# Optimization experiments

Hardware: AMD Instinct MI355X
Metric: run time of the kernel (lower is better)

The kernel has to match this reference:

```python
import jax, jax.numpy as jnp
import numpy as np

B, N, D, E, FF_MULT = 2, 1024, 1024, 8, 4
H = D * FF_MULT


def setup_inputs() -> dict:
    key = jax.random.key(0)
    k = jax.random.split(key, 6)
    tokens = jax.random.normal(k[0], (B, N, D), dtype=jnp.float32)
    # uniform(0,1): strictly positive -> every expert processes every token
    dispatch_weights = jax.random.uniform(k[1], (B, N, E), dtype=jnp.float32)
    combine_weights = jax.random.uniform(k[2], (B, N, E), dtype=jnp.float32)
    # per-expert SwiGLU params, stacked on leading expert axis.
    # stored pre-transposed: y = x @ W  (torch Linear weight is [out,in])
    xavier_dh = np.sqrt(2.0 / (D + H))
    Wg = jax.random.normal(k[3], (E, D, H), dtype=jnp.float32) * xavier_dh
    Wv = jax.random.normal(k[4], (E, D, H), dtype=jnp.float32) * xavier_dh
    Wo = jax.random.normal(k[5], (E, H, D), dtype=jnp.float32) * (0.02 * xavier_dh)
    scale = jnp.full((E,), 1.0 / E, dtype=jnp.float32)  # output_scale init 1/E
    return {"tokens": tokens, "dispatch_weights": dispatch_weights,
            "combine_weights": combine_weights, "Wg": Wg, "Wv": Wv,
            "Wo": Wo, "scale": scale}


def reference(tokens, dispatch_weights, combine_weights, Wg, Wv, Wo, scale):
    b, n, d = tokens.shape
    x = tokens.reshape(b * n, d)                      # (T, D)
    disp = dispatch_weights.reshape(b * n, E)         # (T, E)
    comb = combine_weights.reshape(b * n, E)          # (T, E)
    # SwiGLU FFN for all experts at once (dense grouped GEMM)
    gate = jax.nn.gelu(jnp.einsum('td,edh->teh', x, Wg), approximate=False)
    value = jnp.einsum('td,edh->teh', x, Wv)
    expert_out = jnp.einsum('teh,ehd->ted', gate * value, Wo)  # (T, E, D)
    expert_out = expert_out * scale[None, :, None]
    # combine: weight by combine_weights where dispatched (dispatch > 0)
    w = jnp.where(disp > 0, comb, 0.0)                # (T, E)
    output = jnp.einsum('ted,te->td', expert_out, w)
    return output.reshape(b, n, d)
```

## Files before the change

### kernel.cpp

```cpp
#include <hip/hip_runtime.h>
#include <math.h>

#define T_TOK 2048
#define DDIM 1024
#define HDIM 4096
#define NEXP 8
#define NPRIME 8192
#define KTOT (NEXP * HDIM)
#define NSPLIT 8

typedef unsigned short u16;
typedef __attribute__((ext_vector_type(4))) float f32x4;
typedef __attribute__((ext_vector_type(8))) __bf16 bf16x8;
typedef __attribute__((ext_vector_type(8))) unsigned short u16x8;
typedef __attribute__((ext_vector_type(4))) unsigned short u16x4;

__device__ __forceinline__ u16 f2bf(float f) {
  unsigned int u = __builtin_bit_cast(unsigned int, f);
  u += 0x7fffu + ((u >> 16) & 1u);
  return (u16)(u >> 16);
}

__device__ __forceinline__ void stage16(const u16* g, u16* l) {
  __builtin_amdgcn_global_load_lds((__attribute__((address_space(1))) void*)g,
                                   (__attribute__((address_space(3))) void*)l,
                                   16, 0, 0);
}

__global__ void cvt_x_kernel(const float* __restrict__ x, u16* __restrict__ xb) {
  int i = (blockIdx.x * 256 + threadIdx.x) * 8;
  float4 a = *(const float4*)(x + i);
  float4 b = *(const float4*)(x + i + 4);
  u16x8 o;
  o[0] = f2bf(a.x); o[1] = f2bf(a.y); o[2] = f2bf(a.z); o[3] = f2bf(a.w);
  o[4] = f2bf(b.x); o[5] = f2bf(b.y); o[6] = f2bf(b.z); o[7] = f2bf(b.w);
  *(u16x8*)(xb + i) = o;
}

__global__ void transpose_all_kernel(const float* __restrict__ Wg,
                                     const float* __restrict__ Wv,
                                     const float* __restrict__ Wo,
                                     u16* __restrict__ wgvT, u16* __restrict__ woT2) {
  __shared__ float lds[64][65];
  const int bid = blockIdx.x;
  const int e = bid / 3072;
  const int r = bid % 3072;
  const int which = r >> 10;
  const int tt = r & 1023;
  const float* src; int R, C;
  if (which == 2) { src = Wo + (size_t)e * HDIM * DDIM; R = HDIM; C = DDIM; }
  else            { src = (which ? Wv : Wg) + (size_t)e * DDIM * HDIM; R = DDIM; C = HDIM; }
  const int nrt = R >> 6;
  const int r0 = (tt % nrt) << 6, c0 = (tt / nrt) << 6;
  const int tid = threadIdx.x;
#pragma unroll
  for (int i = 0; i < 4; ++i) {
    int f4 = tid + 256 * i;
    int row = f4 >> 4, c4 = (f4 & 15) << 2;
    float4 v = *(const float4*)(src + (size_t)(r0 + row) * C + c0 + c4);
    lds[row][c4] = v.x; lds[row][c4 + 1] = v.y; lds[row][c4 + 2] = v.z; lds[row][c4 + 3] = v.w;
  }
  __syncthreads();
#pragma unroll
  for (int i = 0; i < 4; ++i) {
    int f4 = tid + 256 * i;
    int cc = f4 >> 4, r4 = (f4 & 15) << 2;
    u16x4 o;
    o[0] = f2bf(lds[r4][cc]);     o[1] = f2bf(lds[r4 + 1][cc]);
    o[2] = f2bf(lds[r4 + 2][cc]); o[3] = f2bf(lds[r4 + 3][cc]);
    u16* dst;
    if (which == 2) {
      dst = woT2 + (size_t)(c0 + cc) * KTOT + e * HDIM + r0 + r4;
    } else {
      int h = c0 + cc;
      int rowp = ((h >> 4) << 5) + which * 16 + (h & 15);
      dst = wgvT + (size_t)e * NPRIME * DDIM + (size_t)rowp * DDIM + r0 + r4;
    }
    *(u16x4*)dst = o;
  }
}


template<int KS>
__device__ __forceinline__ void stageA_half(const u16* Ab, int Am0, int tk,
                                            u16* slot, int tid, int h) {
#pragma unroll
  for (int i = 0; i < 2; ++i) {
    int ca = tid + i * 512;
    int rowi = ca >> 3, sl = ca & 7;
    int row = (rowi & 63) + h * 64 + (rowi >> 6) * 128;
    const u16* g = Ab + (size_t)(Am0 + row) * KS + tk + ((sl ^ (row & 7)) << 3);
    stage16(g, slot + ((row << 3) + sl) * 8);
  }
}
template<int KS>
__device__ __forceinline__ void stageB_full(const u16* Bb, int Bn0, int tk,
                                            u16* slot, int tid) {
#pragma unroll
  for (int i = 0; i < 4; ++i) {
    int cb = tid + i * 512;
    int row = cb >> 3, sl = cb & 7;
    const u16* g = Bb + (size_t)(Bn0 + row) * KS + tk + ((sl ^ (row & 7)) << 3);
    stage16(g, slot + 16384 + cb * 8);
  }
}

__device__ __forceinline__ bf16x8 ldsA(const u16* slot, int row, int j, int lkq) {
  int sl = ((j << 2) | lkq) ^ (row & 7);
  return *(const bf16x8*)(slot + row * 64 + sl * 8);
}
__device__ __forceinline__ bf16x8 ldsB(const u16* slot, int row, int j, int lkq) {
  int sl = ((j << 2) | lkq) ^ (row & 7);
  return *(const bf16x8*)(slot + 16384 + row * 64 + sl * 8);
}

template<int KS>
__device__ __forceinline__ void gemm_loop(const u16* Ab, const u16* Bb,
                                          int Am0, int Bn0, int kbase, int NT,
                                          u16* lds, int tid, f32x4 (&acc)[8][4]) {
  const int lane = tid & 63;
  const int wave = tid >> 6;
  const int wm = wave >> 2;
  const int wn = wave & 3;
  const int l15 = lane & 15;
  const int lkq = lane >> 4;

  u16* slot0 = lds;
  u16* slot1 = lds + 32768;

  stageA_half<KS>(Ab, Am0, kbase, slot0, tid, 0);
  stageA_half<KS>(Ab, Am0, kbase, slot0, tid, 1);
  stageB_full<KS>(Bb, Bn0, kbase, slot0, tid);
  stageA_half<KS>(Ab, Am0, kbase + 64, slot1, tid, 0);
  asm volatile("s_waitcnt vmcnt(2)" ::: "memory");
  asm volatile("s_barrier" ::: "memory");

#pragma unroll 1
  for (int t = 0; t < NT; ++t) {
    u16* s  = lds + (t & 1) * 32768;
    u16* s2 = lds + ((t & 1) ^ 1) * 32768;
    bf16x8 af[4], bfr[2][4];

    if (t + 1 < NT) {
      stageA_half<KS>(Ab, Am0, kbase + (t + 1) * 64, s2, tid, 1);
      stageB_full<KS>(Bb, Bn0, kbase + (t + 1) * 64, s2, tid);
    }
#pragma unroll
    for (int mf = 0; mf < 4; ++mf) af[mf] = ldsA(s, wm * 128 + mf * 16 + l15, 0, lkq);
#pragma unroll
    for (int nf = 0; nf < 4; ++nf) bfr[0][nf] = ldsB(s, wn * 64 + nf * 16 + l15, 0, lkq);
    __builtin_amdgcn_s_setprio(1);
#pragma unroll
    for (int mf = 0; mf < 4; ++mf)
#pragma unroll
      for (int nf = 0; nf < 4; ++nf)
        acc[mf][nf] = __builtin_amdgcn_mfma_f32_16x16x32_bf16(af[mf], bfr[0][nf], acc[mf][nf], 0, 0, 0);
    __builtin_amdgcn_s_setprio(0);
    asm volatile("s_barrier" ::: "memory");

#pragma unroll
    for (int mf = 0; mf < 4; ++mf) af[mf] = ldsA(s, wm * 128 + 64 + mf * 16 + l15, 0, lkq);
    __builtin_amdgcn_s_setprio(1);
#pragma unroll
    for (int mf = 0; mf < 4; ++mf)
#pragma unroll
      for (int nf = 0; nf < 4; ++nf)
        acc[4 + mf][nf] = __builtin_amdgcn_mfma_f32_16x16x32_bf16(af[mf], bfr[0][nf], acc[4 + mf][nf], 0, 0, 0);
    __builtin_amdgcn_s_setprio(0);
    asm volatile("s_barrier" ::: "memory");

#pragma unroll
    for (int mf = 0; mf < 4; ++mf) af[mf] = ldsA(s, wm * 128 + mf * 16 + l15, 1, lkq);
#pragma unroll
    for (int nf = 0; nf < 4; ++nf) bfr[1][nf] = ldsB(s, wn * 64 + nf * 16 + l15, 1, lkq);
    __builtin_amdgcn_s_setprio(1);
#pragma unroll
    for (int mf = 0; mf < 4; ++mf)
#pragma unroll
      for (int nf = 0; nf < 4; ++nf)
        acc[mf][nf] = __builtin_amdgcn_mfma_f32_16x16x32_bf16(af[mf], bfr[1][nf], acc[mf][nf], 0, 0, 0);
    __builtin_amdgcn_s_setprio(0);
    asm volatile("s_barrier" ::: "memory");

    if (t + 2 < NT) stageA_half<KS>(Ab, Am0, kbase + (t + 2) * 64, s, tid, 0);
#pragma unroll
    for (int mf = 0; mf < 4; ++mf) af[mf] = ldsA(s, wm * 128 + 64 + mf * 16 + l15, 1, lkq);
    __builtin_amdgcn_s_setprio(1);
#pragma unroll
    for (int mf = 0; mf < 4; ++mf)
#pragma unroll
      for (int nf = 0; nf < 4; ++nf)
        acc[4 + mf][nf] = __builtin_amdgcn_mfma_f32_16x16x32_bf16(af[mf], bfr[1][nf], acc[4 + mf][nf], 0, 0, 0);
    __builtin_amdgcn_s_setprio(0);
    if (t + 2 < NT)       { asm volatile("s_waitcnt vmcnt(2)" ::: "memory"); }
    else if (t + 2 == NT) { asm volatile("s_waitcnt vmcnt(0)" ::: "memory"); }
    asm volatile("s_barrier" ::: "memory");
  }
}

__global__ void __launch_bounds__(512, 2)
gemm_gv_kernel(const u16* __restrict__ xb, const u16* __restrict__ wgvT,
               const float* __restrict__ disp, const float* __restrict__ comb,
               const float* __restrict__ scale, u16* __restrict__ h) {
  __shared__ u16 lds[65536];

  const int bid = blockIdx.x;
  const int wg = (bid & 7) * 256 + (bid >> 3);
  const int e  = wg >> 8;
  const int rr = wg & 255;
  const int nt = rr >> 3;
  const int mt = rr & 7;

  const int tid = threadIdx.x;
  const int lane = tid & 63;
  const int wave = tid >> 6;
  const int wm = wave >> 2, wn = wave & 3;
  const int l15 = lane & 15, lkq = lane >> 4;

  const u16* Bb = wgvT + (size_t)e * NPRIME * DDIM;
  const int Am0 = mt * 256;
  const int Bn0 = nt * 256;

  f32x4 acc[8][4] = {};
  gemm_loop<DDIM>(xb, Bb, Am0, Bn0, 0, DDIM / 64, lds, tid, acc);

  const float s_e = scale[e];
  const int hbase = nt * 128 + wn * 32;
#pragma unroll
  for (int a = 0; a < 8; ++a) {
#pragma unroll
    for (int r = 0; r < 4; ++r) {
      const int t = Am0 + wm * 128 + a * 16 + lkq * 4 + r;
      const float dv = disp[t * NEXP + e];
      const float cv = comb[t * NEXP + e];
      const float s = (dv > 0.0f) ? cv * s_e : 0.0f;
#pragma unroll
      for (int jj = 0; jj < 2; ++jj) {
        const float g = acc[a][2 * jj][r];
        const float v = acc[a][2 * jj + 1][r];
        const float ge = 0.5f * g * (1.0f + erff(g * 0.70710678f));
        h[(size_t)t * KTOT + e * HDIM + hbase + jj * 16 + l15] = f2bf(ge * v * s);
      }
    }
  }
}

__global__ void __launch_bounds__(512, 2)
gemm_out_kernel(const u16* __restrict__ hb, const u16* __restrict__ woT2,
                float* __restrict__ P) {
  __shared__ u16 lds[65536];

  const int bid = blockIdx.x;
  const int wg = (bid & 7) * 32 + (bid >> 3);
  const int kz = wg >> 5;
  const int rr = wg & 31;
  const int nt = rr >> 3;
  const int mt = rr & 7;

  const int tid = threadIdx.x;
  const int lane = tid & 63;
  const int wave = tid >> 6;
  const int wm = wave >> 2, wn = wave & 3;
  const int l15 = lane & 15, lkq = lane >> 4;

  const int Am0 = mt * 256;
  const int Bn0 = nt * 256;
  const int kbase = kz * (KTOT / NSPLIT);

  f32x4 acc[8][4] = {};
  gemm_loop<KTOT>(hb, woT2, Am0, Bn0, kbase, (KTOT / NSPLIT) / 64, lds, tid, acc);

  float* Pp = P + (size_t)kz * (T_TOK * DDIM);
#pragma unroll
  for (int a = 0; a < 8; ++a) {
#pragma unroll
    for (int r = 0; r < 4; ++r) {
      const int t = Am0 + wm * 128 + a * 16 + lkq * 4 + r;
#pragma unroll
      for (int nf = 0; nf < 4; ++nf)
        Pp[(size_t)t * DDIM + Bn0 + wn * 64 + nf * 16 + l15] = acc[a][nf][r];
    }
  }
}

__global__ void reduce_out_kernel(const float* __restrict__ P, float* __restrict__ out) {
  int i = blockIdx.x * 256 + threadIdx.x;
  float4 a = ((const float4*)P)[i];
#pragma unroll
  for (int s = 1; s < NSPLIT; ++s) {
    float4 b = ((const float4*)P)[i + s * (T_TOK * DDIM / 4)];
    a.x += b.x; a.y += b.y; a.z += b.z; a.w += b.w;
  }
  ((float4*)out)[i] = a;
}

extern "C" void kernel_launch(void* const* d_in, const int* in_sizes, int n_in,
                              void* d_out, int out_size, void* d_ws, size_t ws_size,
                              hipStream_t stream) {
  const float* tokens = (const float*)d_in[0];
  const float* disp   = (const float*)d_in[1];
  const float* comb   = (const float*)d_in[2];
  const float* Wg     = (const float*)d_in[3];
  const float* Wv     = (const float*)d_in[4];
  const float* Wo     = (const float*)d_in[5];
  const float* scale  = (const float*)d_in[6];
  float* out = (float*)d_out;

  char* ws = (char*)d_ws;
  const size_t MB = 1024 * 1024;
  u16* xb    = (u16*)(ws);
  u16* wgvT  = (u16*)(ws + 4   * MB);
  u16* woT2  = (u16*)(ws + 132 * MB);
  u16* hbuf  = (u16*)(ws + 196 * MB);
  float* P   = (float*)(ws + 324 * MB);

  cvt_x_kernel<<<1024, 256, 0, stream>>>(tokens, xb);
  transpose_all_kernel<<<24576, 256, 0, stream>>>(Wg, Wv, Wo, wgvT, woT2);
  gemm_gv_kernel<<<2048, 512, 0, stream>>>(xb, wgvT, disp, comb, scale, hbuf);
  gemm_out_kernel<<<256, 512, 0, stream>>>(hbuf, woT2, P);
  reduce_out_kernel<<<2048, 256, 0, stream>>>(P, out);
}
```

Baseline: 555.3 us.

## Restructure GEMM main loop into quadrant phases with interleaved async LDS staging

Rewrites the double-buffered GEMM K-loop so each 64-wide K tile is processed in four quadrant phases (A-top/B-left, B-right, A-bottom, and so on). Each phase loads its fragments for both k-substeps at once and issues one quarter of the next tile's global-to-LDS copies. Staging addresses are precomputed per thread, and sched_barrier plus explicit vmcnt/lgkmcnt waits pin the ordering. The aim is to spread memory traffic evenly across the MFMA bursts and cut redundant fragment reloads. The cost is more barriers per iteration and tighter wait-count bookkeeping, which could stall if the counts are wrong.

```diff
diff --git a/kernel.cpp b/kernel.cpp
--- a/kernel.cpp
+++ b/kernel.cpp
@@ -81,30 +81,6 @@
 }
 
 
-template<int KS>
-__device__ __forceinline__ void stageA_half(const u16* Ab, int Am0, int tk,
-                                            u16* slot, int tid, int h) {
-#pragma unroll
-  for (int i = 0; i < 2; ++i) {
-    int ca = tid + i * 512;
-    int rowi = ca >> 3, sl = ca & 7;
-    int row = (rowi & 63) + h * 64 + (rowi >> 6) * 128;
-    const u16* g = Ab + (size_t)(Am0 + row) * KS + tk + ((sl ^ (row & 7)) << 3);
-    stage16(g, slot + ((row << 3) + sl) * 8);
-  }
-}
-template<int KS>
-__device__ __forceinline__ void stageB_full(const u16* Bb, int Bn0, int tk,
-                                            u16* slot, int tid) {
-#pragma unroll
-  for (int i = 0; i < 4; ++i) {
-    int cb = tid + i * 512;
-    int row = cb >> 3, sl = cb & 7;
-    const u16* g = Bb + (size_t)(Bn0 + row) * KS + tk + ((sl ^ (row & 7)) << 3);
-    stage16(g, slot + 16384 + cb * 8);
-  }
-}
-
 __device__ __forceinline__ bf16x8 ldsA(const u16* slot, int row, int j, int lkq) {
   int sl = ((j << 2) | lkq) ^ (row & 7);
   return *(const bf16x8*)(slot + row * 64 + sl * 8);
@@ -120,81 +96,134 @@
                                           u16* lds, int tid, f32x4 (&acc)[8][4]) {
   const int lane = tid & 63;
   const int wave = tid >> 6;
-  const int wm = wave >> 2;
-  const int wn = wave & 3;
-  const int l15 = lane & 15;
-  const int lkq = lane >> 4;
-
-  u16* slot0 = lds;
-  u16* slot1 = lds + 32768;
-
-  stageA_half<KS>(Ab, Am0, kbase, slot0, tid, 0);
-  stageA_half<KS>(Ab, Am0, kbase, slot0, tid, 1);
-  stageB_full<KS>(Bb, Bn0, kbase, slot0, tid);
-  stageA_half<KS>(Ab, Am0, kbase + 64, slot1, tid, 0);
-  asm volatile("s_waitcnt vmcnt(2)" ::: "memory");
-  asm volatile("s_barrier" ::: "memory");
+  const int wm = wave >> 2, wn = wave & 3;
+  const int l15 = lane & 15, lkq = lane >> 4;
+
+  const int sl = tid & 7, rw = tid >> 3;
+  const int slx = (sl ^ (rw & 7)) << 3;
+  const int rb = (rw & 31) + ((rw >> 5) << 6);
+  const u16* pA = Ab + (size_t)(Am0 + rw) * KS + kbase + slx;
+  const u16* pB = Bb + (size_t)(Bn0 + rb) * KS + kbase + slx;
+  const int dA = rw * 64 + sl * 8;
+  const int dB = 16384 + rb * 64 + sl * 8;
+
+  auto SA0 = [&](int k, u16* slot) {
+    stage16(pA + k, slot + dA);
+    stage16(pA + (size_t)128 * KS + k, slot + dA + 128 * 64);
+  };
+  auto SA1 = [&](int k, u16* slot) {
+    stage16(pA + (size_t)64 * KS + k, slot + dA + 64 * 64);
+    stage16(pA + (size_t)192 * KS + k, slot + dA + 192 * 64);
+  };
+  auto SB0 = [&](int k, u16* slot) {
+    stage16(pB + k, slot + dB);
+    stage16(pB + (size_t)128 * KS + k, slot + dB + 128 * 64);
+  };
+  auto SB1 = [&](int k, u16* slot) {
+    stage16(pB + (size_t)32 * KS + k, slot + dB + 32 * 64);
+    stage16(pB + (size_t)160 * KS + k, slot + dB + 160 * 64);
+  };
+
+  SA0(0, lds); SB0(0, lds); SB1(0, lds); SA1(0, lds);
+  asm volatile("s_waitcnt vmcnt(4)" ::: "memory");
+  __builtin_amdgcn_s_barrier();
 
 #pragma unroll 1
   for (int t = 0; t < NT; ++t) {
     u16* s  = lds + (t & 1) * 32768;
     u16* s2 = lds + ((t & 1) ^ 1) * 32768;
-    bf16x8 af[4], bfr[2][4];
-
-    if (t + 1 < NT) {
-      stageA_half<KS>(Ab, Am0, kbase + (t + 1) * 64, s2, tid, 1);
-      stageB_full<KS>(Bb, Bn0, kbase + (t + 1) * 64, s2, tid);
-    }
-#pragma unroll
-    for (int mf = 0; mf < 4; ++mf) af[mf] = ldsA(s, wm * 128 + mf * 16 + l15, 0, lkq);
-#pragma unroll
-    for (int nf = 0; nf < 4; ++nf) bfr[0][nf] = ldsB(s, wn * 64 + nf * 16 + l15, 0, lkq);
+    const int kn = (t + 1) << 6;
+    const bool more = (t + 1 < NT);
+    bf16x8 af[4][2], bfr[4][2];
+
+#pragma unroll
+    for (int mf = 0; mf < 4; ++mf)
+#pragma unroll
+      for (int ks = 0; ks < 2; ++ks)
+        af[mf][ks] = ldsA(s, wm * 128 + mf * 16 + l15, ks, lkq);
+#pragma unroll
+    for (int nf = 0; nf < 2; ++nf)
+#pragma unroll
+      for (int ks = 0; ks < 2; ++ks)
+        bfr[nf][ks] = ldsB(s, wn * 64 + nf * 16 + l15, ks, lkq);
+    if (more) SA0(kn, s2);
+    __builtin_amdgcn_sched_barrier(0);
+    __builtin_amdgcn_s_barrier();
+    asm volatile("s_waitcnt lgkmcnt(0)" ::: "memory");
+    __builtin_amdgcn_sched_barrier(0);
     __builtin_amdgcn_s_setprio(1);
 #pragma unroll
+    for (int ks = 0; ks < 2; ++ks)
+#pragma unroll
+      for (int mf = 0; mf < 4; ++mf)
+#pragma unroll
+        for (int nf = 0; nf < 2; ++nf)
+          acc[mf][nf] = __builtin_amdgcn_mfma_f32_16x16x32_bf16(af[mf][ks], bfr[nf][ks], acc[mf][nf], 0, 0, 0);
+    __builtin_amdgcn_s_setprio(0);
+    if (more) { asm volatile("s_waitcnt vmcnt(4)" ::: "memory"); }
+    else      { asm volatile("s_waitcnt vmcnt(2)" ::: "memory"); }
+    __builtin_amdgcn_s_barrier();
+    __builtin_amdgcn_sched_barrier(0);
+
+#pragma unroll
+    for (int nf = 2; nf < 4; ++nf)
+#pragma unroll
+      for (int ks = 0; ks < 2; ++ks)
+        bfr[nf][ks] = ldsB(s, wn * 64 + nf * 16 + l15, ks, lkq);
+    if (more) SB0(kn, s2);
+    __builtin_amdgcn_sched_barrier(0);
+    __builtin_amdgcn_s_barrier();
+    asm volatile("s_waitcnt lgkmcnt(0)" ::: "memory");
+    __builtin_amdgcn_sched_barrier(0);
+    __builtin_amdgcn_s_setprio(1);
+#pragma unroll
+    for (int ks = 0; ks < 2; ++ks)
+#pragma unroll
+      for (int mf = 0; mf < 4; ++mf)
+#pragma unroll
+        for (int nf = 2; nf < 4; ++nf)
+          acc[mf][nf] = __builtin_amdgcn_mfma_f32_16x16x32_bf16(af[mf][ks], bfr[nf][ks], acc[mf][nf], 0, 0, 0);
+    __builtin_amdgcn_s_setprio(0);
+    if (more) { asm volatile("s_waitcnt vmcnt(4)" ::: "memory"); }
+    else      { asm volatile("s_waitcnt vmcnt(0)" ::: "memory"); }
+    __builtin_amdgcn_s_barrier();
+    __builtin_amdgcn_sched_barrier(0);
+
+#pragma unroll
     for (int mf = 0; mf < 4; ++mf)
 #pragma unroll
-      for (int nf = 0; nf < 4; ++nf)
-        acc[mf][nf] = __builtin_amdgcn_mfma_f32_16x16x32_bf16(af[mf], bfr[0][nf], acc[mf][nf], 0, 0, 0);
+      for (int ks = 0; ks < 2; ++ks)
+        af[mf][ks] = ldsA(s, wm * 128 + 64 + mf * 16 + l15, ks, lkq);
+    if (more) SB1(kn, s2);
+    __builtin_amdgcn_sched_barrier(0);
+    __builtin_amdgcn_s_barrier();
+    asm volatile("s_waitcnt lgkmcnt(0)" ::: "memory");
+    __builtin_amdgcn_sched_barrier(0);
+    __builtin_amdgcn_s_setprio(1);
+#pragma unroll
+    for (int ks = 0; ks < 2; ++ks)
+#pragma unroll
+      for (int mf = 0; mf < 4; ++mf)
+#pragma unroll
+        for (int nf = 0; nf < 2; ++nf)
+          acc[4 + mf][nf] = __builtin_amdgcn_mfma_f32_16x16x32_bf16(af[mf][ks], bfr[nf][ks], acc[4 + mf][nf], 0, 0, 0);
     __builtin_amdgcn_s_setprio(0);
-    asm volatile("s_barrier" ::: "memory");
-
-#pragma unroll
-    for (int mf = 0; mf < 4; ++mf) af[mf] = ldsA(s, wm * 128 + 64 + mf * 16 + l15, 0, lkq);
+    __builtin_amdgcn_s_barrier();
+    __builtin_amdgcn_sched_barrier(0);
+
+    if (more) SA1(kn, s2);
     __builtin_amdgcn_s_setprio(1);
 #pragma unroll
-    for (int mf = 0; mf < 4; ++mf)
-#pragma unroll
-      for (int nf = 0; nf < 4; ++nf)
-        acc[4 + mf][nf] = __builtin_amdgcn_mfma_f32_16x16x32_bf16(af[mf], bfr[0][nf], acc[4 + mf][nf], 0, 0, 0);
+    for (int ks = 0; ks < 2; ++ks)
+#pragma unroll
+      for (int mf = 0; mf < 4; ++mf)
+#pragma unroll
+        for (int nf = 2; nf < 4; ++nf)
+          acc[4 + mf][nf] = __builtin_amdgcn_mfma_f32_16x16x32_bf16(af[mf][ks], bfr[nf][ks], acc[4 + mf][nf], 0, 0, 0);
     __builtin_amdgcn_s_setprio(0);
-    asm volatile("s_barrier" ::: "memory");
-
-#pragma unroll
-    for (int mf = 0; mf < 4; ++mf) af[mf] = ldsA(s, wm * 128 + mf * 16 + l15, 1, lkq);
-#pragma unroll
-    for (int nf = 0; nf < 4; ++nf) bfr[1][nf] = ldsB(s, wn * 64 + nf * 16 + l15, 1, lkq);
-    __builtin_amdgcn_s_setprio(1);
-#pragma unroll
-    for (int mf = 0; mf < 4; ++mf)
-#pragma unroll
-      for (int nf = 0; nf < 4; ++nf)
-        acc[mf][nf] = __builtin_amdgcn_mfma_f32_16x16x32_bf16(af[mf], bfr[1][nf], acc[mf][nf], 0, 0, 0);
-    __builtin_amdgcn_s_setprio(0);
-    asm volatile("s_barrier" ::: "memory");
-
-    if (t + 2 < NT) stageA_half<KS>(Ab, Am0, kbase + (t + 2) * 64, s, tid, 0);
-#pragma unroll
-    for (int mf = 0; mf < 4; ++mf) af[mf] = ldsA(s, wm * 128 + 64 + mf * 16 + l15, 1, lkq);
-    __builtin_amdgcn_s_setprio(1);
-#pragma unroll
-    for (int mf = 0; mf < 4; ++mf)
-#pragma unroll
-      for (int nf = 0; nf < 4; ++nf)
-        acc[4 + mf][nf] = __builtin_amdgcn_mfma_f32_16x16x32_bf16(af[mf], bfr[1][nf], acc[4 + mf][nf], 0, 0, 0);
-    __builtin_amdgcn_s_setprio(0);
-    if (t + 2 < NT)       { asm volatile("s_waitcnt vmcnt(2)" ::: "memory"); }
-    else if (t + 2 == NT) { asm volatile("s_waitcnt vmcnt(0)" ::: "memory"); }
-    asm volatile("s_barrier" ::: "memory");
+    if (more) { asm volatile("s_waitcnt vmcnt(4)" ::: "memory"); }
+    __builtin_amdgcn_s_barrier();
+    __builtin_amdgcn_sched_barrier(0);
   }
 }
 
```

After: 555.2 us. About the same (-0.0%).

## Rework GEMM main loop into 4-stage BK=32 pipeline with register prefetch

Applied to the files above, without the earlier changes.

Replaces the double-buffered BK=64 K loop with a four-slot ring of BK=32 tiles, each staged three iterations ahead. A and B fragments for the next tile are read from LDS while the current MFMAs run. Barriers drop from four to two per iteration, and the LDS swizzle changes to suit 32-wide rows. The aim is to hide global and LDS latency better, at the cost of more iterations, more registers, and hand-tuned waitcnt values that must exactly match the number of loads in flight.

```diff
diff --git a/kernel.cpp b/kernel.cpp
--- a/kernel.cpp
+++ b/kernel.cpp
@@ -82,119 +82,100 @@
 
 
 template<int KS>
-__device__ __forceinline__ void stageA_half(const u16* Ab, int Am0, int tk,
-                                            u16* slot, int tid, int h) {
-#pragma unroll
-  for (int i = 0; i < 2; ++i) {
-    int ca = tid + i * 512;
-    int rowi = ca >> 3, sl = ca & 7;
-    int row = (rowi & 63) + h * 64 + (rowi >> 6) * 128;
-    const u16* g = Ab + (size_t)(Am0 + row) * KS + tk + ((sl ^ (row & 7)) << 3);
-    stage16(g, slot + ((row << 3) + sl) * 8);
-  }
-}
-template<int KS>
-__device__ __forceinline__ void stageB_full(const u16* Bb, int Bn0, int tk,
-                                            u16* slot, int tid) {
-#pragma unroll
-  for (int i = 0; i < 4; ++i) {
-    int cb = tid + i * 512;
-    int row = cb >> 3, sl = cb & 7;
-    const u16* g = Bb + (size_t)(Bn0 + row) * KS + tk + ((sl ^ (row & 7)) << 3);
-    stage16(g, slot + 16384 + cb * 8);
-  }
-}
-
-__device__ __forceinline__ bf16x8 ldsA(const u16* slot, int row, int j, int lkq) {
-  int sl = ((j << 2) | lkq) ^ (row & 7);
-  return *(const bf16x8*)(slot + row * 64 + sl * 8);
-}
-__device__ __forceinline__ bf16x8 ldsB(const u16* slot, int row, int j, int lkq) {
-  int sl = ((j << 2) | lkq) ^ (row & 7);
-  return *(const bf16x8*)(slot + 16384 + row * 64 + sl * 8);
-}
-
-template<int KS>
 __device__ __forceinline__ void gemm_loop(const u16* Ab, const u16* Bb,
                                           int Am0, int Bn0, int kbase, int NT,
                                           u16* lds, int tid, f32x4 (&acc)[8][4]) {
   const int lane = tid & 63;
   const int wave = tid >> 6;
-  const int wm = wave >> 2;
-  const int wn = wave & 3;
-  const int l15 = lane & 15;
-  const int lkq = lane >> 4;
-
-  u16* slot0 = lds;
-  u16* slot1 = lds + 32768;
-
-  stageA_half<KS>(Ab, Am0, kbase, slot0, tid, 0);
-  stageA_half<KS>(Ab, Am0, kbase, slot0, tid, 1);
-  stageB_full<KS>(Bb, Bn0, kbase, slot0, tid);
-  stageA_half<KS>(Ab, Am0, kbase + 64, slot1, tid, 0);
-  asm volatile("s_waitcnt vmcnt(2)" ::: "memory");
-  asm volatile("s_barrier" ::: "memory");
+  const int wm = wave >> 2, wn = wave & 3;
+  const int l15 = lane & 15, lkq = lane >> 4;
+
+  const int cA0 = tid, cA1 = tid + 512;
+  auto srcA = [&](int c) {
+    int row = c >> 2, s = c & 3;
+    int sx = s ^ (row & 3) ^ ((row >> 2) & 3);
+    return Ab + (size_t)(Am0 + row) * KS + kbase + (sx << 3);
+  };
+  auto srcB = [&](int c) {
+    int row = c >> 2, s = c & 3;
+    int sx = s ^ (row & 3) ^ ((row >> 2) & 3);
+    return Bb + (size_t)(Bn0 + row) * KS + kbase + (sx << 3);
+  };
+  const u16* gA0 = srcA(cA0); const u16* gA1 = srcA(cA1);
+  const u16* gB0 = srcB(cA0); const u16* gB1 = srcB(cA1);
+
+  auto stageA = [&](int t) {
+    u16* sl_ = lds + ((t & 3) << 14);
+    int k0 = t << 5;
+    stage16(gA0 + k0, sl_ + cA0 * 8);
+    stage16(gA1 + k0, sl_ + cA1 * 8);
+  };
+  auto stageB = [&](int t) {
+    u16* sl_ = lds + ((t & 3) << 14);
+    int k0 = t << 5;
+    stage16(gB0 + k0, sl_ + 8192 + cA0 * 8);
+    stage16(gB1 + k0, sl_ + 8192 + cA1 * 8);
+  };
+
+  auto ldA = [&](const u16* sl_, int mf) -> bf16x8 {
+    int row = wm * 128 + mf * 16 + l15;
+    int s = lkq ^ (row & 3) ^ ((row >> 2) & 3);
+    return *(const bf16x8*)(sl_ + row * 32 + s * 8);
+  };
+  auto ldB = [&](const u16* sl_, int nf) -> bf16x8 {
+    int row = wn * 64 + nf * 16 + l15;
+    int s = lkq ^ (row & 3) ^ ((row >> 2) & 3);
+    return *(const bf16x8*)(sl_ + 8192 + row * 32 + s * 8);
+  };
+
+  bf16x8 af[8], bf[4], bfn[4];
+
+  stageA(0); stageB(0); stageA(1); stageB(1); stageA(2); stageB(2);
+  asm volatile("s_waitcnt vmcnt(4)" ::: "memory");
+  __builtin_amdgcn_s_barrier();
+#pragma unroll
+  for (int mf = 0; mf < 4; ++mf) af[mf] = ldA(lds, mf);
+#pragma unroll
+  for (int nf = 0; nf < 4; ++nf) bf[nf] = ldB(lds, nf);
 
 #pragma unroll 1
   for (int t = 0; t < NT; ++t) {
-    u16* s  = lds + (t & 1) * 32768;
-    u16* s2 = lds + ((t & 1) ^ 1) * 32768;
-    bf16x8 af[4], bfr[2][4];
-
-    if (t + 1 < NT) {
-      stageA_half<KS>(Ab, Am0, kbase + (t + 1) * 64, s2, tid, 1);
-      stageB_full<KS>(Bb, Bn0, kbase + (t + 1) * 64, s2, tid);
-    }
-#pragma unroll
-    for (int mf = 0; mf < 4; ++mf) af[mf] = ldsA(s, wm * 128 + mf * 16 + l15, 0, lkq);
-#pragma unroll
-    for (int nf = 0; nf < 4; ++nf) bfr[0][nf] = ldsB(s, wn * 64 + nf * 16 + l15, 0, lkq);
+    u16* sc = lds + ((t & 3) << 14);
+    const int tn = (t + 1 < NT) ? t + 1 : t;
+    u16* sn = lds + ((tn & 3) << 14);
+
+#pragma unroll
+    for (int mf = 0; mf < 4; ++mf) af[4 + mf] = ldA(sc, 4 + mf);
+    bfn[0] = ldB(sn, 0); bfn[1] = ldB(sn, 1);
+    if (t + 3 < NT) stageA(t + 3);
+    asm volatile("s_waitcnt lgkmcnt(6)" ::: "memory");
+    __builtin_amdgcn_sched_barrier(0);
     __builtin_amdgcn_s_setprio(1);
 #pragma unroll
     for (int mf = 0; mf < 4; ++mf)
 #pragma unroll
       for (int nf = 0; nf < 4; ++nf)
-        acc[mf][nf] = __builtin_amdgcn_mfma_f32_16x16x32_bf16(af[mf], bfr[0][nf], acc[mf][nf], 0, 0, 0);
+        acc[mf][nf] = __builtin_amdgcn_mfma_f32_16x16x32_bf16(af[mf], bf[nf], acc[mf][nf], 0, 0, 0);
     __builtin_amdgcn_s_setprio(0);
-    asm volatile("s_barrier" ::: "memory");
-
-#pragma unroll
-    for (int mf = 0; mf < 4; ++mf) af[mf] = ldsA(s, wm * 128 + 64 + mf * 16 + l15, 0, lkq);
+    __builtin_amdgcn_s_barrier();
+
+    bfn[2] = ldB(sn, 2); bfn[3] = ldB(sn, 3);
+#pragma unroll
+    for (int mf = 0; mf < 4; ++mf) af[mf] = ldA(sn, mf);
+    if (t + 3 < NT) stageB(t + 3);
+    asm volatile("s_waitcnt lgkmcnt(6)" ::: "memory");
+    __builtin_amdgcn_sched_barrier(0);
     __builtin_amdgcn_s_setprio(1);
 #pragma unroll
     for (int mf = 0; mf < 4; ++mf)
 #pragma unroll
       for (int nf = 0; nf < 4; ++nf)
-        acc[4 + mf][nf] = __builtin_amdgcn_mfma_f32_16x16x32_bf16(af[mf], bfr[0][nf], acc[4 + mf][nf], 0, 0, 0);
+        acc[4 + mf][nf] = __builtin_amdgcn_mfma_f32_16x16x32_bf16(af[4 + mf], bf[nf], acc[4 + mf][nf], 0, 0, 0);
     __builtin_amdgcn_s_setprio(0);
-    asm volatile("s_barrier" ::: "memory");
-
-#pragma unroll
-    for (int mf = 0; mf < 4; ++mf) af[mf] = ldsA(s, wm * 128 + mf * 16 + l15, 1, lkq);
-#pragma unroll
-    for (int nf = 0; nf < 4; ++nf) bfr[1][nf] = ldsB(s, wn * 64 + nf * 16 + l15, 1, lkq);
-    __builtin_amdgcn_s_setprio(1);
-#pragma unroll
-    for (int mf = 0; mf < 4; ++mf)
-#pragma unroll
-      for (int nf = 0; nf < 4; ++nf)
-        acc[mf][nf] = __builtin_amdgcn_mfma_f32_16x16x32_bf16(af[mf], bfr[1][nf], acc[mf][nf], 0, 0, 0);
-    __builtin_amdgcn_s_setprio(0);
-    asm volatile("s_barrier" ::: "memory");
-
-    if (t + 2 < NT) stageA_half<KS>(Ab, Am0, kbase + (t + 2) * 64, s, tid, 0);
-#pragma unroll
-    for (int mf = 0; mf < 4; ++mf) af[mf] = ldsA(s, wm * 128 + 64 + mf * 16 + l15, 1, lkq);
-    __builtin_amdgcn_s_setprio(1);
-#pragma unroll
-    for (int mf = 0; mf < 4; ++mf)
-#pragma unroll
-      for (int nf = 0; nf < 4; ++nf)
-        acc[4 + mf][nf] = __builtin_amdgcn_mfma_f32_16x16x32_bf16(af[mf], bfr[1][nf], acc[4 + mf][nf], 0, 0, 0);
-    __builtin_amdgcn_s_setprio(0);
-    if (t + 2 < NT)       { asm volatile("s_waitcnt vmcnt(2)" ::: "memory"); }
-    else if (t + 2 == NT) { asm volatile("s_waitcnt vmcnt(0)" ::: "memory"); }
-    asm volatile("s_barrier" ::: "memory");
+    if (t + 3 < NT) { asm volatile("s_waitcnt vmcnt(4)" ::: "memory"); }
+    else            { asm volatile("s_waitcnt vmcnt(0)" ::: "memory"); }
+    __builtin_amdgcn_s_barrier();
+    bf[0] = bfn[0]; bf[1] = bfn[1]; bf[2] = bfn[2]; bf[3] = bfn[3];
   }
 }
 
@@ -222,7 +203,7 @@
   const int Bn0 = nt * 256;
 
   f32x4 acc[8][4] = {};
-  gemm_loop<DDIM>(xb, Bb, Am0, Bn0, 0, DDIM / 64, lds, tid, acc);
+  gemm_loop<DDIM>(xb, Bb, Am0, Bn0, 0, DDIM / 32, lds, tid, acc);
 
   const float s_e = scale[e];
   const int hbase = nt * 128 + wn * 32;
@@ -268,7 +249,7 @@
   const int kbase = kz * (KTOT / NSPLIT);
 
   f32x4 acc[8][4] = {};
-  gemm_loop<KTOT>(hb, woT2, Am0, Bn0, kbase, (KTOT / NSPLIT) / 64, lds, tid, acc);
+  gemm_loop<KTOT>(hb, woT2, Am0, Bn0, kbase, (KTOT / NSPLIT) / 32, lds, tid, acc);
 
   float* Pp = P + (size_t)kz * (T_TOK * DDIM);
 #pragma unroll
```

Measured after the change: 600.7 us. 1.08x slower.
